# Performance work log

Measured on AMD Instinct MI355X. Metric: run time of the kernel, lower is better.

## Reference

```python
import jax, jax.numpy as jnp
import numpy as np

NUM_HEADS = 16
HEAD_DIM = 128  # 2048 / 16


def setup_inputs() -> dict:
    key = jax.random.key(0)
    ks = jax.random.split(key, 5)
    B, S, D = 2, 2048, 2048
    scale = 1.0 / np.sqrt(D)
    return {
        "x": jax.random.normal(ks[0], (B, S, D), dtype=jnp.float32),
        "Wq": jax.random.normal(ks[1], (D, D), dtype=jnp.float32) * scale,
        "Wk": jax.random.normal(ks[2], (D, D), dtype=jnp.float32) * scale,
        "Wv": jax.random.normal(ks[3], (D, D), dtype=jnp.float32) * scale,
        "Wo": jax.random.normal(ks[4], (D, D), dtype=jnp.float32) * scale,
    }


def reference(x, Wq, Wk, Wv, Wo):
    B, S, D = x.shape
    H, Hd = NUM_HEADS, HEAD_DIM
    # nn.Linear(bias=False): y = x @ W.T
    q = (x @ Wq.T).reshape(B, S, H, Hd).transpose(0, 2, 1, 3)  # [B,H,S,Hd]
    k = (x @ Wk.T).reshape(B, S, H, Hd).transpose(0, 2, 1, 3)
    v = (x @ Wv.T).reshape(B, S, H, Hd).transpose(0, 2, 1, 3)
    scores = jnp.einsum("bhqd,bhkd->bhqk", q, k) / jnp.sqrt(jnp.float32(Hd))
    attn = jax.nn.softmax(scores, axis=-1)  # dropout p=0 (eval) -> identity
    out = jnp.einsum("bhqk,bhkd->bhqd", attn, v)  # [B,H,S,Hd]
    out = out.transpose(0, 2, 1, 3).reshape(B, S, D)
    out = out @ Wo.T
    return out
```

## Files before the change

### kernel.cpp

```cpp
#include <hip/hip_runtime.h>
#include <math.h>
#include <stdint.h>


#define DDIM 2048
#define SEQ  2048
#define NH   16
#define HD   128

typedef __attribute__((ext_vector_type(4))) float f32x4;
typedef __attribute__((ext_vector_type(16))) float f32x16;
typedef __attribute__((ext_vector_type(8))) __bf16 bf16x8;
typedef __attribute__((ext_vector_type(4))) unsigned int u32x4;
typedef __attribute__((ext_vector_type(2))) unsigned int u32x2;

#define MFMA_B16(a, b, c) __builtin_amdgcn_mfma_f32_16x16x32_bf16((a), (b), (c), 0, 0, 0)
#define MFMA32(a, b, c) __builtin_amdgcn_mfma_f32_32x32x16_bf16((a), (b), (c), 0, 0, 0)

__device__ __forceinline__ void async16(const void* g, void* l) {
  __builtin_amdgcn_global_load_lds(
      (const __attribute__((address_space(1))) unsigned int*)g,
      (__attribute__((address_space(3))) unsigned int*)l, 16, 0, 0);
}

__device__ __forceinline__ unsigned short f2bf(float f) {
  unsigned u = __builtin_bit_cast(unsigned, f);
  u += 0x7fffu + ((u >> 16) & 1u);
  return (unsigned short)(u >> 16);
}

__device__ __forceinline__ bf16x8 ldfrag(const unsigned short* p) {
  return __builtin_bit_cast(bf16x8, *(const u32x4*)p);
}

__device__ __forceinline__ void cvt_body(const float* __restrict__ s,
                                         unsigned short* __restrict__ d, int i) {
  const f32x4* sp = (const f32x4*)s;
  f32x4 a = sp[2 * i], b = sp[2 * i + 1];
  u32x4 o;
  o.x = ((unsigned)f2bf(a.y) << 16) | f2bf(a.x);
  o.y = ((unsigned)f2bf(a.w) << 16) | f2bf(a.z);
  o.z = ((unsigned)f2bf(b.y) << 16) | f2bf(b.x);
  o.w = ((unsigned)f2bf(b.w) << 16) | f2bf(b.z);
  ((u32x4*)d)[i] = o;
}

__global__ __launch_bounds__(256) void cvt_bf16_kernel(const float* __restrict__ s,
                                                       unsigned short* __restrict__ d) {
  cvt_body(s, d, blockIdx.x * 256 + threadIdx.x);
}

__global__ __launch_bounds__(256) void cvt_all_kernel(const float* __restrict__ x,
                                                      const float* __restrict__ wq,
                                                      const float* __restrict__ wk,
                                                      const float* __restrict__ wv,
                                                      unsigned short* __restrict__ xb,
                                                      unsigned short* __restrict__ wqkv) {
  const int b = blockIdx.x;
  if (b < 4096) {
    cvt_body(x, xb, b * 256 + threadIdx.x);
  } else {
    const int wi = (b - 4096) >> 11, lb = (b - 4096) & 2047;
    const float* s = (wi == 0) ? wq : (wi == 1) ? wk : wv;
    cvt_body(s, wqkv + (size_t)wi * 4194304u, lb * 256 + threadIdx.x);
  }
}

template <int MODE>
__global__ __launch_bounds__(256) void gemm32(const unsigned short* __restrict__ A,
                                              const unsigned short* __restrict__ B,
                                              unsigned short* __restrict__ Oqk,
                                              unsigned short* __restrict__ Ovt,
                                              float* __restrict__ Cf, float alpha_q) {
  __shared__ unsigned short As[128 * 64];
  __shared__ unsigned short Bs[128 * 64];
  const int tid = threadIdx.x;
  const int lane = tid & 63, w = tid >> 6;
  const int l32 = lane & 31, half = lane >> 5;
  const int wm = (w >> 1) * 64, wn = (w & 1) * 64;
  const int bm = blockIdx.y * 128, bn = blockIdx.x * 128;

  f32x16 acc[2][2];
#pragma unroll
  for (int i = 0; i < 2; ++i)
#pragma unroll
    for (int j = 0; j < 2; ++j)
#pragma unroll
      for (int e = 0; e < 16; ++e) acc[i][j][e] = 0.f;

  const unsigned short* pa[4];
  const unsigned short* pbb[4];
  {
    const int cg = (tid & 7) ^ ((tid >> 3) & 7);
#pragma unroll
    for (int j = 0; j < 4; ++j) {
      const int row = j * 32 + (tid >> 3);
      pa[j] = A + (size_t)(bm + row) * DDIM + cg * 8;
      pbb[j] = B + (size_t)(bn + row) * DDIM + cg * 8;
    }
  }

  for (int kt = 0; kt < DDIM / 64; ++kt) {
    __syncthreads();
#pragma unroll
    for (int j = 0; j < 4; ++j) {
      async16(pa[j], &As[(j * 256 + tid) * 8]);
      pa[j] += 64;
      async16(pbb[j], &Bs[(j * 256 + tid) * 8]);
      pbb[j] += 64;
    }
    __syncthreads();
#pragma unroll
    for (int ks = 0; ks < 4; ++ks) {
      const int sl = ((ks * 2 + half) ^ (l32 & 7)) * 8;
      bf16x8 af0 = ldfrag(&As[(wm + l32) * 64 + sl]);
      bf16x8 af1 = ldfrag(&As[(wm + 32 + l32) * 64 + sl]);
      bf16x8 bf0 = ldfrag(&Bs[(wn + l32) * 64 + sl]);
      bf16x8 bf1 = ldfrag(&Bs[(wn + 32 + l32) * 64 + sl]);
      acc[0][0] = MFMA32(af0, bf0, acc[0][0]);
      acc[0][1] = MFMA32(af0, bf1, acc[0][1]);
      acc[1][0] = MFMA32(af1, bf0, acc[1][0]);
      acc[1][1] = MFMA32(af1, bf1, acc[1][1]);
    }
  }

  const int seg = (MODE == 0) ? (bn >> 11) : 0;
  const int bnl = bn & 2047;
  const float alpha = (MODE == 0 && seg == 0) ? alpha_q : 1.0f;
#pragma unroll
  for (int i = 0; i < 2; ++i) {
#pragma unroll
    for (int j = 0; j < 2; ++j) {
#pragma unroll
      for (int rg = 0; rg < 4; ++rg) {
        const int m0 = bm + wm + i * 32 + rg * 8 + half * 4;
        const float v0 = acc[i][j][rg * 4 + 0] * alpha;
        const float v1 = acc[i][j][rg * 4 + 1] * alpha;
        const float v2 = acc[i][j][rg * 4 + 2] * alpha;
        const float v3 = acc[i][j][rg * 4 + 3] * alpha;
        if (MODE == 1) {
          const int n = bn + wn + j * 32 + l32;
          Cf[(size_t)(m0 + 0) * DDIM + n] = v0;
          Cf[(size_t)(m0 + 1) * DDIM + n] = v1;
          Cf[(size_t)(m0 + 2) * DDIM + n] = v2;
          Cf[(size_t)(m0 + 3) * DDIM + n] = v3;
        } else {
          const int n = bnl + wn + j * 32 + l32;
          if (seg < 2) {
            unsigned short* O = Oqk + (size_t)seg * (4096u * 2048u);
            O[(size_t)(m0 + 0) * DDIM + n] = f2bf(v0);
            O[(size_t)(m0 + 1) * DDIM + n] = f2bf(v1);
            O[(size_t)(m0 + 2) * DDIM + n] = f2bf(v2);
            O[(size_t)(m0 + 3) * DDIM + n] = f2bf(v3);
          } else {
            const int bb = m0 >> 11, s0 = m0 & 2047;
            const int hh = n >> 7, dd = n & 127;
            u32x2 st;
            st.x = ((unsigned)f2bf(v1) << 16) | f2bf(v0);
            st.y = ((unsigned)f2bf(v3) << 16) | f2bf(v2);
            *(u32x2*)&Ovt[((size_t)((bb * NH + hh) * HD + dd)) * SEQ + s0] = st;
          }
        }
      }
    }
  }
}

__global__ __launch_bounds__(256) void attn_kernel(const unsigned short* __restrict__ qb,
                                                   const unsigned short* __restrict__ kb,
                                                   const unsigned short* __restrict__ vtb,
                                                   unsigned short* __restrict__ ab) {
  __shared__ unsigned short Ks[64 * 128];
  __shared__ unsigned short Vts[128 * 64];
  __shared__ unsigned short Pw[4 * 16 * 40];
  const int tid = threadIdx.x;
  const int w = tid >> 6, lane = tid & 63;
  const int quad = lane >> 4, l16 = lane & 15;
  const int qt = blockIdx.x, bh = blockIdx.y;
  const int b = bh >> 4, h = bh & 15;
  const int qrow = qt * 64 + w * 16 + l16;

  const unsigned short* qp = qb + ((size_t)(b * SEQ + qrow)) * DDIM + h * HD;
  bf16x8 qf[4];
#pragma unroll
  for (int ks = 0; ks < 4; ++ks) qf[ks] = ldfrag(qp + ks * 32 + quad * 8);

  f32x4 ot[8];
#pragma unroll
  for (int i = 0; i < 8; i++) ot[i] = f32x4{0.f, 0.f, 0.f, 0.f};
  float sumacc = 0.f;

  const unsigned short* kp[4];
  const unsigned short* vp[4];
  {
    const size_t kbase = ((size_t)(b * SEQ)) * DDIM + h * HD;
    const size_t vbase = ((size_t)((b * NH + h) * HD)) * SEQ;
#pragma unroll
    for (int j = 0; j < 4; ++j) {
      const int key = j * 16 + (tid >> 4), cgk = (tid & 15) ^ (key & 15);
      kp[j] = kb + kbase + (size_t)key * DDIM + cgk * 8;
      const int dd = j * 32 + (tid >> 3), cgv = (tid & 7) ^ ((tid >> 3) & 7);
      vp[j] = vtb + vbase + (size_t)dd * SEQ + cgv * 8;
    }
  }
  unsigned short* pw = &Pw[w * 640];

  for (int kt = 0; kt < SEQ / 64; ++kt) {
    __syncthreads();
#pragma unroll
    for (int j = 0; j < 4; ++j) {
      async16(kp[j], &Ks[(j * 256 + tid) * 8]);
      kp[j] += (size_t)64 * DDIM;
      async16(vp[j], &Vts[(j * 256 + tid) * 8]);
      vp[j] += 64;
    }
    __syncthreads();
    f32x4 s[4];
#pragma unroll
    for (int t = 0; t < 4; ++t) s[t] = f32x4{0.f, 0.f, 0.f, 0.f};
#pragma unroll
    for (int ks = 0; ks < 4; ++ks) {
      const int sl = ((ks * 4 + quad) ^ l16) * 8;
#pragma unroll
      for (int t = 0; t < 4; ++t) {
        bf16x8 a = ldfrag(&Ks[(t * 16 + l16) * 128 + sl]);
        s[t] = MFMA_B16(a, qf[ks], s[t]);
      }
    }
    f32x4 p[4];
#pragma unroll
    for (int t = 0; t < 4; ++t) {
      p[t].x = __builtin_amdgcn_exp2f(s[t].x);
      p[t].y = __builtin_amdgcn_exp2f(s[t].y);
      p[t].z = __builtin_amdgcn_exp2f(s[t].z);
      p[t].w = __builtin_amdgcn_exp2f(s[t].w);
      sumacc += (p[t].x + p[t].y) + (p[t].z + p[t].w);
    }
    bf16x8 pb0, pb1;
    {
      u32x2 w0, w1;
      w0.x = ((unsigned)f2bf(p[0].y) << 16) | f2bf(p[0].x);
      w0.y = ((unsigned)f2bf(p[0].w) << 16) | f2bf(p[0].z);
      w1.x = ((unsigned)f2bf(p[1].y) << 16) | f2bf(p[1].x);
      w1.y = ((unsigned)f2bf(p[1].w) << 16) | f2bf(p[1].z);
      *(u32x2*)&pw[l16 * 40 + quad * 4] = w0;
      *(u32x2*)&pw[l16 * 40 + 16 + quad * 4] = w1;
      asm volatile("s_waitcnt lgkmcnt(0)" ::: "memory");
      pb0 = ldfrag(&pw[l16 * 40 + quad * 8]);
      w0.x = ((unsigned)f2bf(p[2].y) << 16) | f2bf(p[2].x);
      w0.y = ((unsigned)f2bf(p[2].w) << 16) | f2bf(p[2].z);
      w1.x = ((unsigned)f2bf(p[3].y) << 16) | f2bf(p[3].x);
      w1.y = ((unsigned)f2bf(p[3].w) << 16) | f2bf(p[3].z);
      *(u32x2*)&pw[l16 * 40 + quad * 4] = w0;
      *(u32x2*)&pw[l16 * 40 + 16 + quad * 4] = w1;
      asm volatile("s_waitcnt lgkmcnt(0)" ::: "memory");
      pb1 = ldfrag(&pw[l16 * 40 + quad * 8]);
    }
#pragma unroll
    for (int mt = 0; mt < 8; ++mt) {
      bf16x8 vf0 = ldfrag(&Vts[(mt * 16 + l16) * 64 + (quad ^ (l16 & 7)) * 8]);
      ot[mt] = MFMA_B16(vf0, pb0, ot[mt]);
      bf16x8 vf1 = ldfrag(&Vts[(mt * 16 + l16) * 64 + ((4 + quad) ^ (l16 & 7)) * 8]);
      ot[mt] = MFMA_B16(vf1, pb1, ot[mt]);
    }
  }
  float total = sumacc;
  total += __shfl_xor(total, 16);
  total += __shfl_xor(total, 32);
  const float inv = 1.0f / total;
  unsigned short* op = ab + ((size_t)(b * SEQ + qrow)) * DDIM + h * HD;
#pragma unroll
  for (int mt = 0; mt < 8; ++mt) {
    f32x4 v = ot[mt] * inv;
    u32x2 st;
    st.x = ((unsigned)f2bf(v.y) << 16) | f2bf(v.x);
    st.y = ((unsigned)f2bf(v.w) << 16) | f2bf(v.z);
    *(u32x2*)&op[mt * 16 + quad * 4] = st;
  }
}

extern "C" void kernel_launch(void* const* d_in, const int* in_sizes, int n_in,
                              void* d_out, int out_size, void* d_ws, size_t ws_size,
                              hipStream_t stream) {
  (void)in_sizes; (void)n_in; (void)out_size; (void)ws_size;
  const float* x = (const float*)d_in[0];
  const float* Wq = (const float*)d_in[1];
  const float* Wk = (const float*)d_in[2];
  const float* Wv = (const float*)d_in[3];
  const float* Wo = (const float*)d_in[4];

  char* ws = (char*)d_ws;
  unsigned short* xb = (unsigned short*)(ws);
  unsigned short* wqkv = (unsigned short*)(ws + 16777216);
  unsigned short* qb = (unsigned short*)(ws + 41943040);
  unsigned short* kb = (unsigned short*)(ws + 58720256);
  unsigned short* vtb = (unsigned short*)(ws + 75497472);

  const float alpha_q = 1.44269504088896341f / sqrtf(128.0f);

  cvt_all_kernel<<<dim3(10240), 256, 0, stream>>>(x, Wq, Wk, Wv, xb, wqkv);

  gemm32<0><<<dim3(48, 32), 256, 0, stream>>>(xb, wqkv, qb, vtb, nullptr, alpha_q);
  cvt_bf16_kernel<<<dim3(2048), 256, 0, stream>>>(Wo, wqkv);

  attn_kernel<<<dim3(32, 32), 256, 0, stream>>>(qb, kb, vtb, xb);

  gemm32<1><<<dim3(16, 32), 256, 0, stream>>>(xb, wqkv, nullptr, nullptr, (float*)d_out,
                                              1.0f);
}
```

Before: 397.3 us.

## Enlarge attention blocks, refine GEMM LDS swizzle, fold Wo conversion into prep kernel

The attention kernel now runs 512 threads per block, covering 128 query rows, so each loaded K/V tile is shared by twice as many queries and global traffic drops. The GEMM's LDS XOR swizzle now mixes in higher row bits and uses a different fragment swizzle for the second 32-row half, to reduce bank conflicts. When the workspace is large enough, Wo is converted inside the combined conversion kernel into a separate buffer, which removes one launch. Running 8 waves per block may lower occupancy per CU, and the Wo path now depends on the workspace size.

```diff
diff --git a/kernel.cpp b/kernel.cpp
--- a/kernel.cpp
+++ b/kernel.cpp
@@ -54,15 +54,19 @@
                                                       const float* __restrict__ wq,
                                                       const float* __restrict__ wk,
                                                       const float* __restrict__ wv,
+                                                      const float* __restrict__ wo,
                                                       unsigned short* __restrict__ xb,
-                                                      unsigned short* __restrict__ wqkv) {
+                                                      unsigned short* __restrict__ wqkv,
+                                                      unsigned short* __restrict__ wob) {
   const int b = blockIdx.x;
   if (b < 4096) {
     cvt_body(x, xb, b * 256 + threadIdx.x);
-  } else {
+  } else if (b < 10240) {
     const int wi = (b - 4096) >> 11, lb = (b - 4096) & 2047;
     const float* s = (wi == 0) ? wq : (wi == 1) ? wk : wv;
     cvt_body(s, wqkv + (size_t)wi * 4194304u, lb * 256 + threadIdx.x);
+  } else {
+    cvt_body(wo, wob, (b - 10240) * 256 + threadIdx.x);
   }
 }
 
@@ -91,14 +95,16 @@
   const unsigned short* pa[4];
   const unsigned short* pbb[4];
   {
-    const int cg = (tid & 7) ^ ((tid >> 3) & 7);
 #pragma unroll
     for (int j = 0; j < 4; ++j) {
       const int row = j * 32 + (tid >> 3);
+      const int cg = (tid & 7) ^ (row & 7) ^ ((row >> 3) & 7);
       pa[j] = A + (size_t)(bm + row) * DDIM + cg * 8;
       pbb[j] = B + (size_t)(bn + row) * DDIM + cg * 8;
     }
   }
+
+  const int fr = (l32 & 7) ^ (l32 >> 3);
 
   for (int kt = 0; kt < DDIM / 64; ++kt) {
     __syncthreads();
@@ -112,11 +118,13 @@
     __syncthreads();
 #pragma unroll
     for (int ks = 0; ks < 4; ++ks) {
-      const int sl = ((ks * 2 + half) ^ (l32 & 7)) * 8;
-      bf16x8 af0 = ldfrag(&As[(wm + l32) * 64 + sl]);
-      bf16x8 af1 = ldfrag(&As[(wm + 32 + l32) * 64 + sl]);
-      bf16x8 bf0 = ldfrag(&Bs[(wn + l32) * 64 + sl]);
-      bf16x8 bf1 = ldfrag(&Bs[(wn + 32 + l32) * 64 + sl]);
+      const int ph = ks * 2 + half;
+      const int sl0 = (ph ^ fr) * 8;
+      const int sl1 = (ph ^ fr ^ 4) * 8;
+      bf16x8 af0 = ldfrag(&As[(wm + l32) * 64 + sl0]);
+      bf16x8 af1 = ldfrag(&As[(wm + 32 + l32) * 64 + sl1]);
+      bf16x8 bf0 = ldfrag(&Bs[(wn + l32) * 64 + sl0]);
+      bf16x8 bf1 = ldfrag(&Bs[(wn + 32 + l32) * 64 + sl1]);
       acc[0][0] = MFMA32(af0, bf0, acc[0][0]);
       acc[0][1] = MFMA32(af0, bf1, acc[0][1]);
       acc[1][0] = MFMA32(af1, bf0, acc[1][0]);
@@ -166,19 +174,19 @@
   }
 }
 
-__global__ __launch_bounds__(256) void attn_kernel(const unsigned short* __restrict__ qb,
+__global__ __launch_bounds__(512) void attn_kernel(const unsigned short* __restrict__ qb,
                                                    const unsigned short* __restrict__ kb,
                                                    const unsigned short* __restrict__ vtb,
                                                    unsigned short* __restrict__ ab) {
   __shared__ unsigned short Ks[64 * 128];
   __shared__ unsigned short Vts[128 * 64];
-  __shared__ unsigned short Pw[4 * 16 * 40];
+  __shared__ unsigned short Pw[8 * 16 * 40];
   const int tid = threadIdx.x;
   const int w = tid >> 6, lane = tid & 63;
   const int quad = lane >> 4, l16 = lane & 15;
   const int qt = blockIdx.x, bh = blockIdx.y;
   const int b = bh >> 4, h = bh & 15;
-  const int qrow = qt * 64 + w * 16 + l16;
+  const int qrow = qt * 128 + w * 16 + l16;
 
   const unsigned short* qp = qb + ((size_t)(b * SEQ + qrow)) * DDIM + h * HD;
   bf16x8 qf[4];
@@ -190,16 +198,16 @@
   for (int i = 0; i < 8; i++) ot[i] = f32x4{0.f, 0.f, 0.f, 0.f};
   float sumacc = 0.f;
 
-  const unsigned short* kp[4];
-  const unsigned short* vp[4];
+  const unsigned short* kp[2];
+  const unsigned short* vp[2];
   {
     const size_t kbase = ((size_t)(b * SEQ)) * DDIM + h * HD;
     const size_t vbase = ((size_t)((b * NH + h) * HD)) * SEQ;
 #pragma unroll
-    for (int j = 0; j < 4; ++j) {
-      const int key = j * 16 + (tid >> 4), cgk = (tid & 15) ^ (key & 15);
+    for (int j = 0; j < 2; ++j) {
+      const int key = j * 32 + (tid >> 4), cgk = (tid & 15) ^ (key & 15);
       kp[j] = kb + kbase + (size_t)key * DDIM + cgk * 8;
-      const int dd = j * 32 + (tid >> 3), cgv = (tid & 7) ^ ((tid >> 3) & 7);
+      const int dd = j * 64 + (tid >> 3), cgv = (tid & 7) ^ (dd & 7);
       vp[j] = vtb + vbase + (size_t)dd * SEQ + cgv * 8;
     }
   }
@@ -208,10 +216,10 @@
   for (int kt = 0; kt < SEQ / 64; ++kt) {
     __syncthreads();
 #pragma unroll
-    for (int j = 0; j < 4; ++j) {
-      async16(kp[j], &Ks[(j * 256 + tid) * 8]);
+    for (int j = 0; j < 2; ++j) {
+      async16(kp[j], &Ks[(j * 512 + tid) * 8]);
       kp[j] += (size_t)64 * DDIM;
-      async16(vp[j], &Vts[(j * 256 + tid) * 8]);
+      async16(vp[j], &Vts[(j * 512 + tid) * 8]);
       vp[j] += 64;
     }
     __syncthreads();
@@ -282,7 +290,7 @@
 extern "C" void kernel_launch(void* const* d_in, const int* in_sizes, int n_in,
                               void* d_out, int out_size, void* d_ws, size_t ws_size,
                               hipStream_t stream) {
-  (void)in_sizes; (void)n_in; (void)out_size; (void)ws_size;
+  (void)in_sizes; (void)n_in; (void)out_size;
   const float* x = (const float*)d_in[0];
   const float* Wq = (const float*)d_in[1];
   const float* Wk = (const float*)d_in[2];
@@ -295,16 +303,22 @@
   unsigned short* qb = (unsigned short*)(ws + 41943040);
   unsigned short* kb = (unsigned short*)(ws + 58720256);
   unsigned short* vtb = (unsigned short*)(ws + 75497472);
+  const bool big = ws_size >= 100663296ull;
+  unsigned short* wob = big ? (unsigned short*)(ws + 92274688) : wqkv;
 
   const float alpha_q = 1.44269504088896341f / sqrtf(128.0f);
 
-  cvt_all_kernel<<<dim3(10240), 256, 0, stream>>>(x, Wq, Wk, Wv, xb, wqkv);
-
-  gemm32<0><<<dim3(48, 32), 256, 0, stream>>>(xb, wqkv, qb, vtb, nullptr, alpha_q);
-  cvt_bf16_kernel<<<dim3(2048), 256, 0, stream>>>(Wo, wqkv);
-
-  attn_kernel<<<dim3(32, 32), 256, 0, stream>>>(qb, kb, vtb, xb);
-
-  gemm32<1><<<dim3(16, 32), 256, 0, stream>>>(xb, wqkv, nullptr, nullptr, (float*)d_out,
+  if (big) {
+    cvt_all_kernel<<<dim3(12288), 256, 0, stream>>>(x, Wq, Wk, Wv, Wo, xb, wqkv, wob);
+    gemm32<0><<<dim3(48, 32), 256, 0, stream>>>(xb, wqkv, qb, vtb, nullptr, alpha_q);
+  } else {
+    cvt_all_kernel<<<dim3(10240), 256, 0, stream>>>(x, Wq, Wk, Wv, Wo, xb, wqkv, wob);
+    gemm32<0><<<dim3(48, 32), 256, 0, stream>>>(xb, wqkv, qb, vtb, nullptr, alpha_q);
+    cvt_bf16_kernel<<<dim3(2048), 256, 0, stream>>>(Wo, wob);
+  }
+
+  attn_kernel<<<dim3(16, 32), 512, 0, stream>>>(qb, kb, vtb, xb);
+
+  gemm32<1><<<dim3(16, 32), 256, 0, stream>>>(xb, wob, nullptr, nullptr, (float*)d_out,
                                               1.0f);
 }
```

New measurement: 368.8 us. -7.2%, faster.
